# Performance work log

Hardware: AMD Instinct MI355X
Metric: run time of the kernel (lower is better)

Reference implementation:

```python
import jax, jax.numpy as jnp
import numpy as np

DEPTH, IN_DIM, GRID, HID, BATCH = 3, 256, 64, 128, 4096
BN_EPS = 1e-5

def _lin(key, fi, fo):
    kw, kb = jax.random.split(key)
    bound = 1.0 / np.sqrt(fi)
    w = jax.random.uniform(kw, (fi, fo), jnp.float32, -bound, bound)
    b = jax.random.uniform(kb, (fo,), jnp.float32, -bound, bound)
    return w, b

def setup_inputs() -> dict:
    key = jax.random.key(0)
    ks = jax.random.split(key, 8)
    x = jax.random.normal(ks[0], (BATCH, IN_DIM), jnp.float32)
    fs = jax.random.normal(ks[1], (DEPTH, IN_DIM, GRID, HID), jnp.float32)
    grids = jnp.tile(jnp.linspace(0.0, 1.0, GRID, dtype=jnp.float32)[None, :], (DEPTH, 1))
    w1, b1 = _lin(ks[2], HID, HID * 2)
    w2, b2 = _lin(ks[3], HID * 2, HID)
    w3, b3 = _lin(ks[4], HID, HID // 2)
    w4, b4 = _lin(ks[5], HID // 2, 1)
    return {
        "x": x, "fs": fs, "grids": grids,
        "w1": w1, "b1": b1, "g1": jnp.ones(HID * 2), "be1": jnp.zeros(HID * 2),
        "w2": w2, "b2": b2, "g2": jnp.ones(HID), "be2": jnp.zeros(HID),
        "w3": w3, "b3": b3, "g3": jnp.ones(HID // 2), "be3": jnp.zeros(HID // 2),
        "w4": w4, "b4": b4,
    }

def _bn(a, g, b):
    # BatchNorm1d, training mode: biased batch variance, eps=1e-5
    m = a.mean(0)
    v = a.var(0)
    return (a - m) / jnp.sqrt(v + BN_EPS) * g + b

def reference(x, fs, grids, w1, b1, g1, be1, w2, b2, g2, be2, w3, b3, g3, be3, w4, b4):
    # per-feature min-max normalization over the batch
    zmin = x.min(0)
    zmax = x.max(0)
    z = (x - zmin) / (zmax - zmin + 1e-6)  # (B, I)
    h = jnp.zeros((x.shape[0], fs.shape[-1]), x.dtype)
    for i in range(fs.shape[0]):  # small fixed depth
        Bm = jax.nn.relu(z[:, :, None] - grids[i][None, None, :])  # (B, I, G)
        # fused multiply-reduce over grid AND input dims: (b,i,g) x (i,g,h) -> (b,h)
        h = h + jnp.einsum('big,igh->bh', Bm, fs[i])
    a = _bn(jax.nn.relu(h @ w1 + b1), g1, be1)
    a = _bn(jax.nn.relu(a @ w2 + b2), g2, be2)
    a = _bn(jax.nn.relu(a @ w3 + b3), g3, be3)
    return a @ w4 + b4  # (B, 1)
```

## Files before the change

### kernel.cpp

```cpp
#include <hip/hip_runtime.h>
#include <hip/hip_fp16.h>

#define BATCH 4096
#define IN_DIM 256
#define GRID_N 64
#define HID 128
#define GEMM_GB 256
constexpr float BN_EPS = 1e-5f;

typedef _Float16 h2 __attribute__((ext_vector_type(2)));
__device__ __forceinline__ h2 as_h2(unsigned u){ union {unsigned x; h2 h;} c; c.x = u; return c.h; }

static const size_t O_MMP  = 0;
static const size_t O_P1   = 32768;
static const size_t O_P2   = O_P1 + 524288;
static const size_t O_P3   = O_P2 + 262144;
static const size_t O_SS1  = O_P3 + 131072;
static const size_t O_SS2  = O_SS1 + 2048;
static const size_t O_STB  = O_SS2 + 2048;
static const size_t O_H    = O_STB + (size_t)256*65*128*4;
static const size_t O_A1   = O_H  + (size_t)4096*128*4;
static const size_t O_A2   = O_A1 + (size_t)4096*256*4;
static const size_t O_A3   = O_A2 + (size_t)4096*128*4;

__global__ __launch_bounds__(256) void k_prep(const float* __restrict__ x, const float* __restrict__ fs,
                                              const float* __restrict__ grids,
                                              float* __restrict__ mmp, unsigned* __restrict__ STb){
    const int tid = threadIdx.x;
    const int bid = blockIdx.x;
    if (bid < 16){
        const float* xp = x + (size_t)bid*256*IN_DIM + tid;
        float mn = 1e30f, mx = -1e30f;
        #pragma unroll 8
        for (int r = 0; r < 256; ++r){
            float v = xp[(size_t)r*IN_DIM];
            mn = fminf(mn, v); mx = fmaxf(mx, v);
        }
        mmp[(size_t)bid*512 + tid]       = mn;
        mmp[(size_t)bid*512 + 256 + tid] = mx;
        return;
    }
    const int i = (bid - 16)*2 + (tid >> 7);
    const int h = tid & 127;
    const float* f0 = fs + ((size_t)(0*IN_DIM + i)*GRID_N)*HID + h;
    const float* f1 = fs + ((size_t)(1*IN_DIM + i)*GRID_N)*HID + h;
    const float* f2 = fs + ((size_t)(2*IN_DIM + i)*GRID_N)*HID + h;
    unsigned* st = STb + (size_t)i*65*HID + h;
    float acc1 = 0.f, acc2 = 0.f;
    st[0] = 0u;
    #pragma unroll 4
    for (int k = 0; k < 64; ++k){
        float fv = f0[(size_t)k*HID] + f1[(size_t)k*HID] + f2[(size_t)k*HID];
        float g  = grids[k];
        acc1 += fv;
        acc2  = fmaf(g, fv, acc2);
        __half2 hh = __halves2half2(__float2half_rn(acc1), __float2half_rn(-acc2));
        st[(size_t)(k+1)*HID] = *reinterpret_cast<unsigned*>(&hh);
    }
}

__global__ __launch_bounds__(128) void k_gather(const float* __restrict__ x, const float* __restrict__ mmp,
                                                const unsigned* __restrict__ STb, float* __restrict__ h){
    __shared__ float s_zmin[256], s_inv[256];
    __shared__ uint2 pre[2][256];
    const int tid = threadIdx.x;
    const int b0  = blockIdx.x * 2;

    for (int f = tid; f < 256; f += 128){
        float mn = 1e30f, mx = -1e30f;
        #pragma unroll
        for (int p = 0; p < 16; ++p){
            mn = fminf(mn, mmp[(size_t)p*512 + f]);
            mx = fmaxf(mx, mmp[(size_t)p*512 + 256 + f]);
        }
        s_zmin[f] = mn;
        s_inv[f]  = 1.0f / (mx - mn + 1e-6f);
    }
    __syncthreads();

    for (int idx = tid; idx < 2*256; idx += 128){
        int bl = idx >> 8, i = idx & 255;
        float z = (x[(size_t)(b0 + bl)*IN_DIM + i] - s_zmin[i]) * s_inv[i];
        int K0 = (int)(z * 63.0f) + 1;
        K0 = max(1, min(63, K0));
        unsigned off = ((unsigned)(i*65 + K0)) << 9;
        __half2 zh = __halves2half2(__float2half_rn(z), __float2half_rn(1.0f));
        pre[bl][i] = make_uint2(*reinterpret_cast<unsigned*>(&zh), off);
    }
    __syncthreads();

    const int w  = tid >> 6;
    const int l  = tid & 63;
    const int hl = l & 31;
    const int hi = l >> 5;
    const char* base = (const char*)STb + (size_t)hl * 16;
    const uint2* pp = &pre[w][hi * 128];
    float acc0 = 0.f, acc1 = 0.f, acc2 = 0.f, acc3 = 0.f;
    #pragma unroll 8
    for (int ii = 0; ii < 128; ++ii){
        uint2 p = pp[ii];
        uint4 u = *reinterpret_cast<const uint4*>(base + p.y);
        h2 zz = as_h2(p.x);
        acc0 = __builtin_amdgcn_fdot2(zz, as_h2(u.x), acc0, false);
        acc1 = __builtin_amdgcn_fdot2(zz, as_h2(u.y), acc1, false);
        acc2 = __builtin_amdgcn_fdot2(zz, as_h2(u.z), acc2, false);
        acc3 = __builtin_amdgcn_fdot2(zz, as_h2(u.w), acc3, false);
    }
    acc0 += __shfl(acc0, hl + 32);
    acc1 += __shfl(acc1, hl + 32);
    acc2 += __shfl(acc2, hl + 32);
    acc3 += __shfl(acc3, hl + 32);
    if (hi == 0){
        *reinterpret_cast<float4*>(&h[(size_t)(b0 + w)*HID + 4*hl]) =
            make_float4(acc0, acc1, acc2, acc3);
    }
}

__global__ __launch_bounds__(256) void k_stats(const float* __restrict__ part, float* __restrict__ stats,
                                               int twoN){
    int j = blockIdx.x*256 + threadIdx.x;
    if (j >= twoN) return;
    float s = 0.f;
    #pragma unroll 8
    for (int p = 0; p < GEMM_GB; ++p) s += part[(size_t)p*twoN + j];
    stats[j] = s;
}

template<int BN_IN>
__global__ __launch_bounds__(256) void k_gemm(const float* __restrict__ A, const float* __restrict__ W,
                                              const float* __restrict__ bias,
                                              const float* __restrict__ instats,
                                              const float* __restrict__ gam, const float* __restrict__ bet,
                                              float* __restrict__ C, float* __restrict__ outpart,
                                              int K, int N){
    __shared__ float As[16][64];
    __shared__ float Ws[64][64];
    __shared__ float bnsc[256], bnsh[256];
    __shared__ float red[16][16][8];

    const int tid = threadIdx.x;
    const int n0  = blockIdx.x * 64;
    const int b0  = blockIdx.y * 16;

    if (BN_IN){
        for (int k = tid; k < K; k += 256){
            float m  = instats[k]     * (1.0f/BATCH);
            float v  = instats[K + k] * (1.0f/BATCH) - m*m;
            float rs = rsqrtf(v + BN_EPS);
            float sc = gam[k]*rs;
            bnsc[k] = sc;
            bnsh[k] = fmaf(-m, sc, bet[k]);
        }
        __syncthreads();
    }

    const int nt = tid & 15;
    const int bt = tid >> 4;
    float acc[4] = {0.f, 0.f, 0.f, 0.f};

    for (int kc = 0; kc < K; kc += 64){
        #pragma unroll
        for (int idx = tid; idx < 16*64; idx += 256){
            int r = idx >> 6, k = idx & 63;
            float a = A[(size_t)(b0 + r)*K + kc + k];
            if (BN_IN) a = fmaf(a, bnsc[kc + k], bnsh[kc + k]);
            As[r][k] = a;
        }
        #pragma unroll
        for (int idx = tid; idx < 64*64; idx += 256){
            int k = idx >> 6, n = idx & 63;
            Ws[k][n] = W[(size_t)(kc + k)*N + n0 + n];
        }
        __syncthreads();
        #pragma unroll
        for (int k = 0; k < 64; ++k){
            float4 w = *reinterpret_cast<const float4*>(&Ws[k][nt*4]);
            float a0 = As[bt][k];
            acc[0] = fmaf(a0, w.x, acc[0]); acc[1] = fmaf(a0, w.y, acc[1]);
            acc[2] = fmaf(a0, w.z, acc[2]); acc[3] = fmaf(a0, w.w, acc[3]);
        }
        __syncthreads();
    }

    float vv[4];
    #pragma unroll
    for (int j = 0; j < 4; ++j){
        float v1 = acc[j] + bias[n0 + nt*4 + j];
        vv[j] = fmaxf(v1, 0.f);
    }
    *reinterpret_cast<float4*>(&C[(size_t)(b0 + bt)*N + n0 + nt*4]) =
        make_float4(vv[0], vv[1], vv[2], vv[3]);
    #pragma unroll
    for (int j = 0; j < 4; ++j){
        red[bt][nt][j]   = vv[j];
        red[bt][nt][4+j] = vv[j]*vv[j];
    }
    __syncthreads();
    for (int s = 8; s > 0; s >>= 1){
        if (bt < s){
            #pragma unroll
            for (int f = 0; f < 8; ++f) red[bt][nt][f] += red[bt+s][nt][f];
        }
        __syncthreads();
    }
    if (bt == 0){
        float* op = outpart + (size_t)blockIdx.y*(2*N);
        #pragma unroll
        for (int j = 0; j < 4; ++j){
            op[n0 + nt*4 + j]     = red[0][nt][j];
            op[N + n0 + nt*4 + j] = red[0][nt][4+j];
        }
    }
}

__global__ __launch_bounds__(256) void k_final(const float* __restrict__ A3, const float* __restrict__ p3,
                                               const float* __restrict__ g3, const float* __restrict__ be3,
                                               const float* __restrict__ w4, const float* __restrict__ b4,
                                               float* __restrict__ out){
    __shared__ float psum[2][128];
    __shared__ float sc[64], sh[64];
    const int t = threadIdx.x;
    {
        int j = t & 127, half = t >> 7;
        float s = 0.f;
        #pragma unroll 8
        for (int p = half*128; p < half*128 + 128; ++p) s += p3[(size_t)p*128 + j];
        psum[half][j] = s;
    }
    __syncthreads();
    if (t < 64){
        float s  = psum[0][t]      + psum[1][t];
        float ss = psum[0][64 + t] + psum[1][64 + t];
        float m  = s  * (1.0f/BATCH);
        float v  = ss * (1.0f/BATCH) - m*m;
        float rs = rsqrtf(v + BN_EPS);
        float g  = g3[t]*rs;
        sc[t] = g * w4[t];
        sh[t] = fmaf(-m, g, be3[t]) * w4[t];
    }
    __syncthreads();
    int row = blockIdx.x*256 + t;
    const float* a = A3 + (size_t)row*64;
    float acc = b4[0];
    #pragma unroll
    for (int k = 0; k < 64; ++k){
        acc = fmaf(a[k], sc[k], acc);
        acc += sh[k];
    }
    out[row] = acc;
}

extern "C" void kernel_launch(void* const* d_in, const int* in_sizes, int n_in,
                              void* d_out, int out_size, void* d_ws, size_t ws_size,
                              hipStream_t stream){
    const float* x     = (const float*)d_in[0];
    const float* fs    = (const float*)d_in[1];
    const float* grids = (const float*)d_in[2];
    const float* w1 = (const float*)d_in[3];  const float* b1 = (const float*)d_in[4];
    const float* g1 = (const float*)d_in[5];  const float* be1= (const float*)d_in[6];
    const float* w2 = (const float*)d_in[7];  const float* b2 = (const float*)d_in[8];
    const float* g2 = (const float*)d_in[9];  const float* be2= (const float*)d_in[10];
    const float* w3 = (const float*)d_in[11]; const float* b3 = (const float*)d_in[12];
    const float* g3 = (const float*)d_in[13]; const float* be3= (const float*)d_in[14];
    const float* w4 = (const float*)d_in[15]; const float* b4 = (const float*)d_in[16];
    float* out = (float*)d_out;

    char* ws = (char*)d_ws;
    float* mmp    = (float*)(ws + O_MMP);
    float* p1     = (float*)(ws + O_P1);
    float* p2     = (float*)(ws + O_P2);
    float* p3     = (float*)(ws + O_P3);
    float* ss1    = (float*)(ws + O_SS1);
    float* ss2    = (float*)(ws + O_SS2);
    unsigned* STb = (unsigned*)(ws + O_STB);
    float* h      = (float*)(ws + O_H);
    float* A1     = (float*)(ws + O_A1);
    float* A2     = (float*)(ws + O_A2);
    float* A3     = (float*)(ws + O_A3);

    k_prep<<<144, 256, 0, stream>>>(x, fs, grids, mmp, STb);
    k_gather<<<2048, 128, 0, stream>>>(x, mmp, STb, h);
    k_gemm<0><<<dim3(4, 256), 256, 0, stream>>>(h,  w1, b1, nullptr, nullptr, nullptr, A1, p1, 128, 256);
    k_stats<<<2, 256, 0, stream>>>(p1, ss1, 512);
    k_gemm<1><<<dim3(2, 256), 256, 0, stream>>>(A1, w2, b2, ss1, g1, be1,            A2, p2, 256, 128);
    k_stats<<<1, 256, 0, stream>>>(p2, ss2, 256);
    k_gemm<1><<<dim3(1, 256), 256, 0, stream>>>(A2, w3, b3, ss2, g2, be2,            A3, p3, 128, 64);
    k_final<<<16, 256, 0, stream>>>(A3, p3, g3, be3, w4, b4, out);
}
```

Before: 119.6 us.

## Fuse first dense layer and its BN partial stats into gather kernel

The gather kernel now handles 4 batch rows per 256-thread block, keeps the hidden vector h in shared memory, and computes the first linear layer with bias, ReLU and per-block sum/sumsq partials directly. This removes the h round-trip through global memory and one GEMM launch. The cost is that each block rereads all of w1 (128x256) for only 4 rows, giving low reuse, and the stats reduction now sums 1024 partials instead of 256.

Result: slower. 142.5 us (+19.2%).

```diff
diff --git a/kernel.cpp b/kernel.cpp
--- a/kernel.cpp
+++ b/kernel.cpp
@@ -5,7 +5,6 @@
 #define IN_DIM 256
 #define GRID_N 64
 #define HID 128
-#define GEMM_GB 256
 constexpr float BN_EPS = 1e-5f;
 
 typedef _Float16 h2 __attribute__((ext_vector_type(2)));
@@ -13,13 +12,12 @@
 
 static const size_t O_MMP  = 0;
 static const size_t O_P1   = 32768;
-static const size_t O_P2   = O_P1 + 524288;
+static const size_t O_P2   = O_P1 + 2097152;
 static const size_t O_P3   = O_P2 + 262144;
 static const size_t O_SS1  = O_P3 + 131072;
 static const size_t O_SS2  = O_SS1 + 2048;
-static const size_t O_STB  = O_SS2 + 2048;
-static const size_t O_H    = O_STB + (size_t)256*65*128*4;
-static const size_t O_A1   = O_H  + (size_t)4096*128*4;
+static const size_t O_STB  = O_SS2 + 1024;
+static const size_t O_A1   = O_STB + (size_t)256*65*128*4;
 static const size_t O_A2   = O_A1 + (size_t)4096*256*4;
 static const size_t O_A3   = O_A2 + (size_t)4096*128*4;
 
@@ -59,14 +57,18 @@
     }
 }
 
-__global__ __launch_bounds__(128) void k_gather(const float* __restrict__ x, const float* __restrict__ mmp,
-                                                const unsigned* __restrict__ STb, float* __restrict__ h){
+__global__ __launch_bounds__(256) void k_gather_g1(const float* __restrict__ x, const float* __restrict__ mmp,
+                                                   const unsigned* __restrict__ STb,
+                                                   const float* __restrict__ w1, const float* __restrict__ b1,
+                                                   float* __restrict__ A1, float* __restrict__ p1){
     __shared__ float s_zmin[256], s_inv[256];
-    __shared__ uint2 pre[2][256];
+    __shared__ uint2 pre[4][256];
+    __shared__ float h_lds[4][128];
     const int tid = threadIdx.x;
-    const int b0  = blockIdx.x * 2;
-
-    for (int f = tid; f < 256; f += 128){
+    const int b0  = blockIdx.x * 4;
+
+    {
+        int f = tid;
         float mn = 1e30f, mx = -1e30f;
         #pragma unroll
         for (int p = 0; p < 16; ++p){
@@ -78,7 +80,7 @@
     }
     __syncthreads();
 
-    for (int idx = tid; idx < 2*256; idx += 128){
+    for (int idx = tid; idx < 4*256; idx += 256){
         int bl = idx >> 8, i = idx & 255;
         float z = (x[(size_t)(b0 + bl)*IN_DIM + i] - s_zmin[i]) * s_inv[i];
         int K0 = (int)(z * 63.0f) + 1;
@@ -89,40 +91,62 @@
     }
     __syncthreads();
 
-    const int w  = tid >> 6;
-    const int l  = tid & 63;
-    const int hl = l & 31;
-    const int hi = l >> 5;
-    const char* base = (const char*)STb + (size_t)hl * 16;
-    const uint2* pp = &pre[w][hi * 128];
-    float acc0 = 0.f, acc1 = 0.f, acc2 = 0.f, acc3 = 0.f;
-    #pragma unroll 8
-    for (int ii = 0; ii < 128; ++ii){
-        uint2 p = pp[ii];
-        uint4 u = *reinterpret_cast<const uint4*>(base + p.y);
-        h2 zz = as_h2(p.x);
-        acc0 = __builtin_amdgcn_fdot2(zz, as_h2(u.x), acc0, false);
-        acc1 = __builtin_amdgcn_fdot2(zz, as_h2(u.y), acc1, false);
-        acc2 = __builtin_amdgcn_fdot2(zz, as_h2(u.z), acc2, false);
-        acc3 = __builtin_amdgcn_fdot2(zz, as_h2(u.w), acc3, false);
-    }
-    acc0 += __shfl(acc0, hl + 32);
-    acc1 += __shfl(acc1, hl + 32);
-    acc2 += __shfl(acc2, hl + 32);
-    acc3 += __shfl(acc3, hl + 32);
-    if (hi == 0){
-        *reinterpret_cast<float4*>(&h[(size_t)(b0 + w)*HID + 4*hl]) =
-            make_float4(acc0, acc1, acc2, acc3);
+    {
+        const int w  = tid >> 6;
+        const int l  = tid & 63;
+        const int hl = l & 31;
+        const int hi = l >> 5;
+        const char* base = (const char*)STb + (size_t)hl * 16;
+        const uint2* pp = &pre[w][hi * 128];
+        float acc0 = 0.f, acc1 = 0.f, acc2 = 0.f, acc3 = 0.f;
+        #pragma unroll 8
+        for (int ii = 0; ii < 128; ++ii){
+            uint2 p = pp[ii];
+            uint4 u = *reinterpret_cast<const uint4*>(base + p.y);
+            h2 zz = as_h2(p.x);
+            acc0 = __builtin_amdgcn_fdot2(zz, as_h2(u.x), acc0, false);
+            acc1 = __builtin_amdgcn_fdot2(zz, as_h2(u.y), acc1, false);
+            acc2 = __builtin_amdgcn_fdot2(zz, as_h2(u.z), acc2, false);
+            acc3 = __builtin_amdgcn_fdot2(zz, as_h2(u.w), acc3, false);
+        }
+        acc0 += __shfl(acc0, hl + 32);
+        acc1 += __shfl(acc1, hl + 32);
+        acc2 += __shfl(acc2, hl + 32);
+        acc3 += __shfl(acc3, hl + 32);
+        if (hi == 0){
+            *reinterpret_cast<float4*>(&h_lds[w][4*hl]) = make_float4(acc0, acc1, acc2, acc3);
+        }
+    }
+    __syncthreads();
+
+    {
+        float a0 = 0.f, a1 = 0.f, a2 = 0.f, a3 = 0.f;
+        #pragma unroll 8
+        for (int k = 0; k < 128; ++k){
+            float wv = w1[(size_t)k*256 + tid];
+            float h0 = h_lds[0][k], h1 = h_lds[1][k], h2v = h_lds[2][k], h3 = h_lds[3][k];
+            a0 = fmaf(h0, wv, a0); a1 = fmaf(h1, wv, a1);
+            a2 = fmaf(h2v, wv, a2); a3 = fmaf(h3, wv, a3);
+        }
+        float bb = b1[tid];
+        float v0 = fmaxf(a0 + bb, 0.f), v1 = fmaxf(a1 + bb, 0.f);
+        float v2 = fmaxf(a2 + bb, 0.f), v3 = fmaxf(a3 + bb, 0.f);
+        A1[(size_t)(b0 + 0)*256 + tid] = v0;
+        A1[(size_t)(b0 + 1)*256 + tid] = v1;
+        A1[(size_t)(b0 + 2)*256 + tid] = v2;
+        A1[(size_t)(b0 + 3)*256 + tid] = v3;
+        p1[(size_t)blockIdx.x*512 + tid]       = v0 + v1 + v2 + v3;
+        p1[(size_t)blockIdx.x*512 + 256 + tid] = v0*v0 + v1*v1 + v2*v2 + v3*v3;
     }
 }
 
 __global__ __launch_bounds__(256) void k_stats(const float* __restrict__ part, float* __restrict__ stats,
-                                               int twoN){
+                                               int twoN, int nparts){
     int j = blockIdx.x*256 + threadIdx.x;
     if (j >= twoN) return;
     float s = 0.f;
     #pragma unroll 8
-    for (int p = 0; p < GEMM_GB; ++p) s += part[(size_t)p*twoN + j];
+    for (int p = 0; p < nparts; ++p) s += part[(size_t)p*twoN + j];
     stats[j] = s;
 }
 
@@ -273,17 +297,15 @@
     float* ss1    = (float*)(ws + O_SS1);
     float* ss2    = (float*)(ws + O_SS2);
     unsigned* STb = (unsigned*)(ws + O_STB);
-    float* h      = (float*)(ws + O_H);
     float* A1     = (float*)(ws + O_A1);
     float* A2     = (float*)(ws + O_A2);
     float* A3     = (float*)(ws + O_A3);
 
     k_prep<<<144, 256, 0, stream>>>(x, fs, grids, mmp, STb);
-    k_gather<<<2048, 128, 0, stream>>>(x, mmp, STb, h);
-    k_gemm<0><<<dim3(4, 256), 256, 0, stream>>>(h,  w1, b1, nullptr, nullptr, nullptr, A1, p1, 128, 256);
-    k_stats<<<2, 256, 0, stream>>>(p1, ss1, 512);
-    k_gemm<1><<<dim3(2, 256), 256, 0, stream>>>(A1, w2, b2, ss1, g1, be1,            A2, p2, 256, 128);
-    k_stats<<<1, 256, 0, stream>>>(p2, ss2, 256);
-    k_gemm<1><<<dim3(1, 256), 256, 0, stream>>>(A2, w3, b3, ss2, g2, be2,            A3, p3, 128, 64);
+    k_gather_g1<<<1024, 256, 0, stream>>>(x, mmp, STb, w1, b1, A1, p1);
+    k_stats<<<2, 256, 0, stream>>>(p1, ss1, 512, 1024);
+    k_gemm<1><<<dim3(2, 256), 256, 0, stream>>>(A1, w2, b2, ss1, g1, be1, A2, p2, 256, 128);
+    k_stats<<<1, 256, 0, stream>>>(p2, ss2, 256, 256);
+    k_gemm<1><<<dim3(1, 256), 256, 0, stream>>>(A2, w3, b3, ss2, g2, be2, A3, p3, 128, 64);
     k_final<<<16, 256, 0, stream>>>(A3, p3, g3, be3, w4, b4, out);
 }
```
